# Kernel optimization log

Measured on AMD Instinct MI355X. Metric: run time of the kernel, lower is better.

The kernel has to match this reference:

```python
import jax, jax.numpy as jnp
import numpy as np

B, T, N_POS, N_ACT, H = 256, 512, 128, 32, 512
D = N_POS + N_ACT


def setup_inputs() -> dict:
    key = jax.random.key(0)
    ks = jax.random.split(key, 10)
    s_ih = 1.0 / np.sqrt(H)  # torch LSTMCell default uniform(-1/sqrt(H), 1/sqrt(H))
    xav_hc = np.sqrt(2.0 / (B + H))  # xavier_normal_ on [B,H] h0/c0
    return {
        "observation": jax.random.normal(ks[0], (B, T, N_POS), dtype=jnp.float32),
        "action": jax.random.normal(ks[1], (B, T, N_ACT), dtype=jnp.float32),
        "W_ih": jax.random.uniform(ks[2], (4 * H, D), jnp.float32, -s_ih, s_ih),
        "W_hh": jax.random.uniform(ks[3], (4 * H, H), jnp.float32, -s_ih, s_ih),
        "b_ih": jax.random.uniform(ks[4], (4 * H,), jnp.float32, -s_ih, s_ih),
        "b_hh": jax.random.uniform(ks[5], (4 * H,), jnp.float32, -s_ih, s_ih),
        "W_out": jax.random.uniform(ks[6], (1, H), jnp.float32, -s_ih, s_ih),
        "b_out": jax.random.uniform(ks[7], (1,), jnp.float32, -s_ih, s_ih),
        "h0": jax.random.normal(ks[8], (B, H), dtype=jnp.float32) * xav_hc,
        "c0": jax.random.normal(ks[9], (B, H), dtype=jnp.float32) * xav_hc,
    }


def reference(observation, action, W_ih, W_hh, b_ih, b_hh, W_out, b_out, h0, c0):
    # x: [B,T,D] -> scan over time [T,B,D]
    x = jnp.concatenate([observation, action], axis=-1)
    xs = jnp.transpose(x, (1, 0, 2))
    b = b_ih + b_hh

    def step(carry, x_t):
        h, c = carry
        gates = x_t @ W_ih.T + h @ W_hh.T + b  # [B, 4H]
        i, f, g, o = jnp.split(gates, 4, axis=-1)
        i = jax.nn.sigmoid(i)
        f = jax.nn.sigmoid(f)
        g = jnp.tanh(g)
        o = jax.nn.sigmoid(o)
        c_new = f * c + i * g
        h_new = o * jnp.tanh(c_new)
        y = h_new @ W_out.T + b_out  # [B, 1]
        return (h_new, c_new), y

    _, ys = jax.lax.scan(step, (h0, c0), xs)  # ys: [T, B, 1]
    return jnp.transpose(ys, (1, 0, 2))  # [B, T, 1]
```

## Files before the change

### kernel.cpp

```cpp
#include <hip/hip_runtime.h>
#include <math.h>


namespace {
constexpr int kT = 512, kH = 512;

typedef _Float16 v8h __attribute__((ext_vector_type(8)));
typedef float v4f __attribute__((ext_vector_type(4)));
typedef unsigned long long ull;
typedef ull v2u __attribute__((ext_vector_type(2)));

__device__ __forceinline__ ull ld64sc(const ull* p, bool sys) {
    return sys ? __hip_atomic_load(p, __ATOMIC_RELAXED, __HIP_MEMORY_SCOPE_SYSTEM)
               : __hip_atomic_load(p, __ATOMIC_RELAXED, __HIP_MEMORY_SCOPE_AGENT);
}
__device__ __forceinline__ unsigned ld32sc(const unsigned* p, bool sys) {
    return sys ? __hip_atomic_load(p, __ATOMIC_RELAXED, __HIP_MEMORY_SCOPE_SYSTEM)
               : __hip_atomic_load(p, __ATOMIC_RELAXED, __HIP_MEMORY_SCOPE_AGENT);
}
__device__ __forceinline__ void st32sc(unsigned* p, unsigned v, bool sys) {
    if (sys) __hip_atomic_store(p, v, __ATOMIC_RELAXED, __HIP_MEMORY_SCOPE_SYSTEM);
    else     __hip_atomic_store(p, v, __ATOMIC_RELAXED, __HIP_MEMORY_SCOPE_WORKGROUP);
}
__device__ __forceinline__ unsigned ld_sys32(const unsigned* p) {
    return __hip_atomic_load(p, __ATOMIC_RELAXED, __HIP_MEMORY_SCOPE_SYSTEM);
}

__device__ __forceinline__ float tanhff(float x) {
    return fmaf(-2.0f,
                __builtin_amdgcn_rcpf(__builtin_amdgcn_exp2f(x * 2.885390082f) + 1.0f),
                1.0f);
}

__global__ void lstm_init(const float* __restrict__ h0, _Float16* __restrict__ hfA,
                          unsigned* __restrict__ ctrl) {
    int i = blockIdx.x * blockDim.x + threadIdx.x;
    int bb = i >> 9, j = i & 511;
    int bgrp = bb >> 4, b = bb & 15;
    int ck = j >> 5, jl = j & 31, qf = jl >> 3, e = jl & 7;
    int slot = (qf * 16 + b) ^ ck;
    hfA[bgrp * 8192 + ck * 512 + slot * 8 + e] = (_Float16)h0[i];
    if (i < 1152) ctrl[i] = 0u;
}

__global__ __launch_bounds__(256, 1) void lstm_persist(
    const float* __restrict__ obs, const float* __restrict__ act,
    const float* __restrict__ Wih, const float* __restrict__ Whh,
    const float* __restrict__ bih, const float* __restrict__ bhh,
    const float* __restrict__ Wout, const float* __restrict__ bout_p,
    const float* __restrict__ c0,
    _Float16* __restrict__ hfA, _Float16* __restrict__ hfB,
    unsigned* __restrict__ ctrl, float* __restrict__ out) {

    __shared__ __align__(16) char xbuf[2][5 * 1024];
    __shared__ __align__(16) char hbuf[2][16 * 1024];
    __shared__ float ypart[2][4];
    __shared__ float ytail[2];
    __shared__ int sh_role[3];

    const int tid = threadIdx.x;
    const int w = tid >> 6, ln = tid & 63;
    const int lm = ln & 15, q = ln >> 4;

    unsigned* flags = ctrl;
    unsigned* regcnt = ctrl + 1024;
    unsigned* regtotal = ctrl + 1032;

    if (tid == 0) {
        int x = __builtin_amdgcn_s_getreg(20 | (31 << 11)) & 7;
        unsigned slot = atomicAdd(&regcnt[x], 1u);
        asm volatile("s_waitcnt vmcnt(0)" ::: "memory");
        atomicAdd(regtotal, 1u);
        while (ld_sys32(regtotal) < 256u) __builtin_amdgcn_s_sleep(8);
        unsigned cnt[8];
#pragma unroll
        for (int i = 0; i < 8; ++i) cnt[i] = ld_sys32(&regcnt[i]);
        int pure_base = 0, total_pure = 0, lbase = 0;
        for (int i = 0; i < 8; ++i) {
            if (i < x) { pure_base += cnt[i] >> 4; lbase += cnt[i] & 15; }
            total_pure += cnt[i] >> 4;
        }
        int px16 = (int)(cnt[x] >> 4) * 16;
        int bg, jv, sv;
        if ((int)slot < px16) {
            bg = pure_base + ((int)slot >> 4); jv = slot & 15; sv = 0;
        } else {
            int lr = lbase + ((int)slot - px16);
            bg = total_pure + (lr >> 4); jv = lr & 15; sv = 1;
        }
        sh_role[0] = bg; sh_role[1] = jv; sh_role[2] = sv;
    }
    __syncthreads();
    const int bgrp = sh_role[0], jg = sh_role[1];
    const bool sysS = sh_role[2] != 0;
    const int yb = bgrp * 16 + jg;
    unsigned* myflags = flags + bgrp * 64;

    v8h afrag[2][21];
    {
        const int jj = lm >> 2, gt = lm & 3;
        const float scg = (gt == 2) ? 2.885390082f : -1.442695041f;
#pragma unroll
        for (int ti = 0; ti < 2; ++ti) {
            const int grow = gt * kH + jg * 32 + w * 8 + jj * 2 + ti;
#pragma unroll
            for (int kc = 0; kc < 21; ++kc) {
                const int k0 = kc * 32 + q * 8;
                const float* src = (k0 < 160) ? (Wih + grow * 160 + k0)
                                              : (Whh + (size_t)grow * kH + (k0 - 160));
                float4 A = *(const float4*)src;
                float4 Bv = *(const float4*)(src + 4);
                v8h f;
                f[0] = (_Float16)(A.x * scg);  f[1] = (_Float16)(A.y * scg);
                f[2] = (_Float16)(A.z * scg);  f[3] = (_Float16)(A.w * scg);
                f[4] = (_Float16)(Bv.x * scg); f[5] = (_Float16)(Bv.y * scg);
                f[6] = (_Float16)(Bv.z * scg); f[7] = (_Float16)(Bv.w * scg);
                afrag[ti][kc] = f;
            }
        }
    }
    float biasv[2][4];
    float creg[2];
#pragma unroll
    for (int ti = 0; ti < 2; ++ti) {
        const int jloc = jg * 32 + w * 8 + q * 2 + ti;
#pragma unroll
        for (int g = 0; g < 4; ++g) {
            const float s = (g == 2) ? 2.885390082f : -1.442695041f;
            biasv[ti][g] = (bih[g * kH + jloc] + bhh[g * kH + jloc]) * s;
        }
        creg[ti] = c0[(size_t)(bgrp * 16 + lm) * kH + jloc];
    }

    const float bout0 = bout_p[0];
    const float2 wout2 = *(const float2*)(Wout + 2 * tid);
    float4 wout4 = make_float4(0.f, 0.f, 0.f, 0.f);
    if (tid < 128) wout4 = *(const float4*)(Wout + tid * 4);

    const int st = tid - 96, xb = st & 15, c10 = st >> 4;
    const bool isX = (tid >= 96);
    float4 xr[4];

    auto x_load = [&](int tt) {
        if (isX) {
            const size_t brow = (size_t)(bgrp * 16 + xb) * kT + tt;
            const float* p = (c10 < 8) ? (obs + brow * 128 + c10 * 16)
                                       : (act + brow * 32 + (c10 - 8) * 16);
            xr[0] = *(const float4*)(p);
            xr[1] = *(const float4*)(p + 4);
            xr[2] = *(const float4*)(p + 8);
            xr[3] = *(const float4*)(p + 12);
        }
    };
    auto x_write = [&](char* xbase) {
        if (isX) {
            const int kcx = c10 >> 1;
#pragma unroll
            for (int ii = 0; ii < 2; ++ii) {
                const int qx = (2 * c10 + ii) & 3;
                const int slot = (qx * 16 + xb) ^ kcx;
                float4 a = xr[2 * ii], b = xr[2 * ii + 1];
                v8h f;
                f[0] = (_Float16)a.x; f[1] = (_Float16)a.y;
                f[2] = (_Float16)a.z; f[3] = (_Float16)a.w;
                f[4] = (_Float16)b.x; f[5] = (_Float16)b.y;
                f[6] = (_Float16)b.z; f[7] = (_Float16)b.w;
                *(v8h*)(xbase + kcx * 1024 + slot * 16) = f;
            }
        }
    };

    x_load(0);
    x_write(xbuf[0]);
    x_load(1);
    __syncthreads();

    char* const hfAc = (char*)hfA;
    char* const hfBc = (char*)hfB;

#pragma unroll 1
    for (int t = 0; t < kT; ++t) {
        const char* hsrcB = ((t & 1) ? hfBc : hfAc) + (size_t)bgrp * 16384;
        char* hdstB = ((t & 1) ? hfAc : hfBc) + (size_t)bgrp * 16384;
        const char* xcur = xbuf[t & 1];
        char* hreg = hbuf[t & 1];

        if (t > 0) {
            const unsigned tgt = (unsigned)t;
            const unsigned* fp = myflags + ln;
            unsigned v = ld32sc(fp, sysS);
            while (true) {
                unsigned vn = ld32sc(fp, sysS);
                if (__all((int)(v >= tgt))) break;
                v = vn;
            }
        }

        ull u[8];
#pragma unroll
        for (int k = 0; k < 4; ++k) {
            const ull* sp = (const ull*)(hsrcB + k * 4096 + tid * 16);
            u[2 * k]     = ld64sc(sp, sysS);
            u[2 * k + 1] = ld64sc(sp + 1, sysS);
        }

        v4f a0 = {biasv[0][0], biasv[0][1], biasv[0][2], biasv[0][3]};
        v4f a1 = {biasv[1][0], biasv[1][1], biasv[1][2], biasv[1][3]};
#pragma unroll
        for (int kc = 0; kc < 5; ++kc) {
            v8h bfr = *(const v8h*)(xcur + kc * 1024 + (ln ^ kc) * 16);
            a0 = __builtin_amdgcn_mfma_f32_16x16x32_f16(afrag[0][kc], bfr, a0, 0, 0, 0);
            a1 = __builtin_amdgcn_mfma_f32_16x16x32_f16(afrag[1][kc], bfr, a1, 0, 0, 0);
        }

#pragma unroll
        for (int k = 0; k < 4; ++k) {
            v2u val = {u[2 * k], u[2 * k + 1]};
            *(v2u*)(hreg + k * 4096 + tid * 16) = val;
        }
        if (t < kT - 1) x_write(xbuf[(t + 1) & 1]);
        __syncthreads();

        v4f b0 = {0.f, 0.f, 0.f, 0.f}, b1 = {0.f, 0.f, 0.f, 0.f};
#pragma unroll
        for (int ck = 0; ck < 8; ++ck) {
            v8h bfr = *(const v8h*)(hreg + ck * 1024 + (ln ^ ck) * 16);
            a0 = __builtin_amdgcn_mfma_f32_16x16x32_f16(afrag[0][5 + ck], bfr, a0, 0, 0, 0);
            a1 = __builtin_amdgcn_mfma_f32_16x16x32_f16(afrag[1][5 + ck], bfr, a1, 0, 0, 0);
        }
#pragma unroll
        for (int ck = 8; ck < 16; ++ck) {
            v8h bfr = *(const v8h*)(hreg + ck * 1024 + (ln ^ ck) * 16);
            b0 = __builtin_amdgcn_mfma_f32_16x16x32_f16(afrag[0][5 + ck], bfr, b0, 0, 0, 0);
            b1 = __builtin_amdgcn_mfma_f32_16x16x32_f16(afrag[1][5 + ck], bfr, b1, 0, 0, 0);
        }

        union { unsigned u32; _Float16 h2[2]; } pk;
#pragma unroll
        for (int ti = 0; ti < 2; ++ti) {
            v4f a = ti ? (a1 + b1) : (a0 + b0);
            float iv = __builtin_amdgcn_rcpf(1.0f + __builtin_amdgcn_exp2f(a[0]));
            float fv = __builtin_amdgcn_rcpf(1.0f + __builtin_amdgcn_exp2f(a[1]));
            float gv = fmaf(-2.0f,
                            __builtin_amdgcn_rcpf(__builtin_amdgcn_exp2f(a[2]) + 1.0f),
                            1.0f);
            float ov = __builtin_amdgcn_rcpf(1.0f + __builtin_amdgcn_exp2f(a[3]));
            creg[ti] = fmaf(fv, creg[ti], iv * gv);
            pk.h2[ti] = (_Float16)(ov * tanhff(creg[ti]));
        }
        st32sc((unsigned*)(hdstB + jg * 1024 + (w * 16 + (lm ^ jg)) * 16 + q * 4),
               pk.u32, sysS);

        unsigned yraw = 0;
        if (t > 0) {
            const int k = 2 * tid;
            const int ck = k >> 5, qy = (k >> 3) & 3, e = k & 7;
            const int slot = (qy * 16 + jg) ^ ck;
            yraw = *(const unsigned*)(hreg + ck * 1024 + slot * 16 + e * 2);
        }

        asm volatile("s_waitcnt vmcnt(0)" ::: "memory");
        if (ln == 0) st32sc(myflags + jg * 4 + w, (unsigned)(t + 1), sysS);

        if (t < kT - 2) x_load(t + 2);
        if (t > 0) {
            union { unsigned uu; _Float16 hh[2]; } cv;
            cv.uu = yraw;
            float p = (float)cv.hh[0] * wout2.x + (float)cv.hh[1] * wout2.y;
#pragma unroll
            for (int s = 32; s; s >>= 1) p += __shfl_xor(p, s);
            if (ln == 0) ypart[t & 1][w] = p;
        }
        if (t >= 2 && tid == 64) {
            const float* yp = ypart[(t - 1) & 1];
            out[(size_t)yb * kT + (t - 2)] = bout0 + yp[0] + yp[1] + yp[2] + yp[3];
        }
    }

    if (tid < 64) {
        const unsigned* fp = myflags + ln;
        while (true) {
            unsigned v = ld32sc(fp, sysS);
            if (__all((int)(v >= (unsigned)kT))) break;
            __builtin_amdgcn_s_sleep(1);
        }
    }
    __syncthreads();
    if (tid == 64) {
        const float* yp = ypart[1];
        out[(size_t)yb * kT + (kT - 2)] = bout0 + yp[0] + yp[1] + yp[2] + yp[3];
    }
    if (tid < 128) {
        const int j0 = tid * 4;
        const int ck = j0 >> 5, qf = (j0 >> 3) & 3, e0 = j0 & 7;
        const int slot = (qf * 16 + jg) ^ ck;
        union { ull uu; _Float16 h4[4]; } cv;
        cv.uu = ld64sc((const ull*)(hfAc + (size_t)bgrp * 16384 + ck * 1024 +
                                    slot * 16 + e0 * 2), sysS);
        float p = (float)cv.h4[0] * wout4.x + (float)cv.h4[1] * wout4.y +
                  (float)cv.h4[2] * wout4.z + (float)cv.h4[3] * wout4.w;
#pragma unroll
        for (int s = 32; s; s >>= 1) p += __shfl_xor(p, s);
        if (ln == 0) ytail[w] = p;
    }
    __syncthreads();
    if (tid == 0) out[(size_t)yb * kT + (kT - 1)] = ytail[0] + ytail[1] + bout0;
}

}

extern "C" void kernel_launch(void* const* d_in, const int* in_sizes, int n_in,
                              void* d_out, int out_size, void* d_ws, size_t ws_size,
                              hipStream_t stream) {
    const float* obs  = (const float*)d_in[0];
    const float* act  = (const float*)d_in[1];
    const float* Wih  = (const float*)d_in[2];
    const float* Whh  = (const float*)d_in[3];
    const float* bih  = (const float*)d_in[4];
    const float* bhh  = (const float*)d_in[5];
    const float* Wout = (const float*)d_in[6];
    const float* bout = (const float*)d_in[7];
    const float* h0   = (const float*)d_in[8];
    const float* c0   = (const float*)d_in[9];
    float* out = (float*)d_out;

    char* ws = (char*)d_ws;
    _Float16* hfA = (_Float16*)ws;
    _Float16* hfB = (_Float16*)(ws + 262144);
    unsigned* ctrl = (unsigned*)(ws + 524288);

    lstm_init<<<512, 256, 0, stream>>>(h0, hfA, ctrl);
    lstm_persist<<<256, 256, 0, stream>>>(obs, act, Wih, Whh, bih, bhh, Wout, bout,
                                          c0, hfA, hfB, ctrl, out);
}
```

Measured before the change: 1.327 ms.

## Halve persistent blocks, each computing 64 hidden units per batch group

The persistent LSTM kernel now launches 128 workgroups instead of 256. Each block owns 64 hidden units (four MFMA tiles per wave instead of two) and 8 blocks per batch group instead of 16. This cuts the number of flags polled per step and the number of blocks that must synchronise each timestep, at the cost of double the MFMA work and register pressure per block. The h-state stores become 64-bit, and the output projection is split across two batch rows per block.

```diff
diff --git a/kernel.cpp b/kernel.cpp
--- a/kernel.cpp
+++ b/kernel.cpp
@@ -19,6 +19,10 @@
                : __hip_atomic_load(p, __ATOMIC_RELAXED, __HIP_MEMORY_SCOPE_AGENT);
 }
 __device__ __forceinline__ void st32sc(unsigned* p, unsigned v, bool sys) {
+    if (sys) __hip_atomic_store(p, v, __ATOMIC_RELAXED, __HIP_MEMORY_SCOPE_SYSTEM);
+    else     __hip_atomic_store(p, v, __ATOMIC_RELAXED, __HIP_MEMORY_SCOPE_WORKGROUP);
+}
+__device__ __forceinline__ void st64sc(ull* p, ull v, bool sys) {
     if (sys) __hip_atomic_store(p, v, __ATOMIC_RELAXED, __HIP_MEMORY_SCOPE_SYSTEM);
     else     __hip_atomic_store(p, v, __ATOMIC_RELAXED, __HIP_MEMORY_SCOPE_WORKGROUP);
 }
@@ -55,7 +59,7 @@
     __shared__ __align__(16) char xbuf[2][5 * 1024];
     __shared__ __align__(16) char hbuf[2][16 * 1024];
     __shared__ float ypart[2][4];
-    __shared__ float ytail[2];
+    __shared__ float ytail[4];
     __shared__ int sh_role[3];
 
     const int tid = threadIdx.x;
@@ -71,38 +75,38 @@
         unsigned slot = atomicAdd(&regcnt[x], 1u);
         asm volatile("s_waitcnt vmcnt(0)" ::: "memory");
         atomicAdd(regtotal, 1u);
-        while (ld_sys32(regtotal) < 256u) __builtin_amdgcn_s_sleep(8);
+        while (ld_sys32(regtotal) < 128u) __builtin_amdgcn_s_sleep(8);
         unsigned cnt[8];
 #pragma unroll
         for (int i = 0; i < 8; ++i) cnt[i] = ld_sys32(&regcnt[i]);
         int pure_base = 0, total_pure = 0, lbase = 0;
         for (int i = 0; i < 8; ++i) {
-            if (i < x) { pure_base += cnt[i] >> 4; lbase += cnt[i] & 15; }
-            total_pure += cnt[i] >> 4;
-        }
-        int px16 = (int)(cnt[x] >> 4) * 16;
+            if (i < x) { pure_base += cnt[i] >> 3; lbase += cnt[i] & 7; }
+            total_pure += cnt[i] >> 3;
+        }
+        int px8 = (int)(cnt[x] >> 3) * 8;
         int bg, jv, sv;
-        if ((int)slot < px16) {
-            bg = pure_base + ((int)slot >> 4); jv = slot & 15; sv = 0;
+        if ((int)slot < px8) {
+            bg = pure_base + ((int)slot >> 3); jv = slot & 7; sv = 0;
         } else {
-            int lr = lbase + ((int)slot - px16);
-            bg = total_pure + (lr >> 4); jv = lr & 15; sv = 1;
+            int lr = lbase + ((int)slot - px8);
+            bg = total_pure + (lr >> 3); jv = lr & 7; sv = 1;
         }
         sh_role[0] = bg; sh_role[1] = jv; sh_role[2] = sv;
     }
     __syncthreads();
     const int bgrp = sh_role[0], jg = sh_role[1];
     const bool sysS = sh_role[2] != 0;
-    const int yb = bgrp * 16 + jg;
+    const int yb0 = bgrp * 16 + jg * 2;
     unsigned* myflags = flags + bgrp * 64;
 
-    v8h afrag[2][21];
+    v8h afrag[4][21];
     {
         const int jj = lm >> 2, gt = lm & 3;
         const float scg = (gt == 2) ? 2.885390082f : -1.442695041f;
 #pragma unroll
-        for (int ti = 0; ti < 2; ++ti) {
-            const int grow = gt * kH + jg * 32 + w * 8 + jj * 2 + ti;
+        for (int ti = 0; ti < 4; ++ti) {
+            const int grow = gt * kH + jg * 64 + w * 16 + jj * 4 + ti;
 #pragma unroll
             for (int kc = 0; kc < 21; ++kc) {
                 const int k0 = kc * 32 + q * 8;
@@ -119,11 +123,11 @@
             }
         }
     }
-    float biasv[2][4];
-    float creg[2];
-#pragma unroll
-    for (int ti = 0; ti < 2; ++ti) {
-        const int jloc = jg * 32 + w * 8 + q * 2 + ti;
+    v4f biasv[4];
+    float creg[4];
+#pragma unroll
+    for (int ti = 0; ti < 4; ++ti) {
+        const int jloc = jg * 64 + w * 16 + q * 4 + ti;
 #pragma unroll
         for (int g = 0; g < 4; ++g) {
             const float s = (g == 2) ? 2.885390082f : -1.442695041f;
@@ -133,9 +137,13 @@
     }
 
     const float bout0 = bout_p[0];
-    const float2 wout2 = *(const float2*)(Wout + 2 * tid);
-    float4 wout4 = make_float4(0.f, 0.f, 0.f, 0.f);
-    if (tid < 128) wout4 = *(const float4*)(Wout + tid * 4);
+    const int j0y = (w & 1) * 256 + ln * 4;
+    const int cky = j0y >> 5, jly = j0y & 31;
+    const int oy = cky * 1024 +
+                   ((((jly >> 3) * 16 + (jg * 2 + (w >> 1))) ^ cky) * 16) +
+                   (jly & 7) * 2;
+    const float4 ywt4 = *(const float4*)(Wout + j0y);
+    const float4 wout4 = *(const float4*)(Wout + (tid & 127) * 4);
 
     const int st = tid - 96, xb = st & 15, c10 = st >> 4;
     const bool isX = (tid >= 96);
@@ -178,6 +186,10 @@
     char* const hfAc = (char*)hfA;
     char* const hfBc = (char*)hfB;
 
+    const int ckp = jg * 2 + (w >> 1);
+    const int qfp = (w & 1) * 2 + (q >> 1);
+    const int pofs = ckp * 1024 + (((qfp * 16 + lm) ^ ckp) * 16) + (q & 1) * 8;
+
 #pragma unroll 1
     for (int t = 0; t < kT; ++t) {
         const char* hsrcB = ((t & 1) ? hfBc : hfAc) + (size_t)bgrp * 16384;
@@ -187,7 +199,7 @@
 
         if (t > 0) {
             const unsigned tgt = (unsigned)t;
-            const unsigned* fp = myflags + ln;
+            const unsigned* fp = myflags + (ln & 31);
             unsigned v = ld32sc(fp, sysS);
             while (true) {
                 unsigned vn = ld32sc(fp, sysS);
@@ -204,13 +216,19 @@
             u[2 * k + 1] = ld64sc(sp + 1, sysS);
         }
 
-        v4f a0 = {biasv[0][0], biasv[0][1], biasv[0][2], biasv[0][3]};
-        v4f a1 = {biasv[1][0], biasv[1][1], biasv[1][2], biasv[1][3]};
+        v4f aacc[4], bacc[4];
+#pragma unroll
+        for (int ti = 0; ti < 4; ++ti) {
+            aacc[ti] = biasv[ti];
+            bacc[ti] = v4f{0.f, 0.f, 0.f, 0.f};
+        }
 #pragma unroll
         for (int kc = 0; kc < 5; ++kc) {
             v8h bfr = *(const v8h*)(xcur + kc * 1024 + (ln ^ kc) * 16);
-            a0 = __builtin_amdgcn_mfma_f32_16x16x32_f16(afrag[0][kc], bfr, a0, 0, 0, 0);
-            a1 = __builtin_amdgcn_mfma_f32_16x16x32_f16(afrag[1][kc], bfr, a1, 0, 0, 0);
+#pragma unroll
+            for (int ti = 0; ti < 4; ++ti)
+                aacc[ti] = __builtin_amdgcn_mfma_f32_16x16x32_f16(
+                    afrag[ti][kc], bfr, aacc[ti], 0, 0, 0);
         }
 
 #pragma unroll
@@ -221,24 +239,26 @@
         if (t < kT - 1) x_write(xbuf[(t + 1) & 1]);
         __syncthreads();
 
-        v4f b0 = {0.f, 0.f, 0.f, 0.f}, b1 = {0.f, 0.f, 0.f, 0.f};
-#pragma unroll
-        for (int ck = 0; ck < 8; ++ck) {
+#pragma unroll
+        for (int ck = 0; ck < 16; ++ck) {
             v8h bfr = *(const v8h*)(hreg + ck * 1024 + (ln ^ ck) * 16);
-            a0 = __builtin_amdgcn_mfma_f32_16x16x32_f16(afrag[0][5 + ck], bfr, a0, 0, 0, 0);
-            a1 = __builtin_amdgcn_mfma_f32_16x16x32_f16(afrag[1][5 + ck], bfr, a1, 0, 0, 0);
-        }
-#pragma unroll
-        for (int ck = 8; ck < 16; ++ck) {
-            v8h bfr = *(const v8h*)(hreg + ck * 1024 + (ln ^ ck) * 16);
-            b0 = __builtin_amdgcn_mfma_f32_16x16x32_f16(afrag[0][5 + ck], bfr, b0, 0, 0, 0);
-            b1 = __builtin_amdgcn_mfma_f32_16x16x32_f16(afrag[1][5 + ck], bfr, b1, 0, 0, 0);
-        }
-
-        union { unsigned u32; _Float16 h2[2]; } pk;
-#pragma unroll
-        for (int ti = 0; ti < 2; ++ti) {
-            v4f a = ti ? (a1 + b1) : (a0 + b0);
+            if (ck < 8) {
+#pragma unroll
+                for (int ti = 0; ti < 4; ++ti)
+                    aacc[ti] = __builtin_amdgcn_mfma_f32_16x16x32_f16(
+                        afrag[ti][5 + ck], bfr, aacc[ti], 0, 0, 0);
+            } else {
+#pragma unroll
+                for (int ti = 0; ti < 4; ++ti)
+                    bacc[ti] = __builtin_amdgcn_mfma_f32_16x16x32_f16(
+                        afrag[ti][5 + ck], bfr, bacc[ti], 0, 0, 0);
+            }
+        }
+
+        union { ull u64; _Float16 h4[4]; } pk;
+#pragma unroll
+        for (int ti = 0; ti < 4; ++ti) {
+            v4f a = aacc[ti] + bacc[ti];
             float iv = __builtin_amdgcn_rcpf(1.0f + __builtin_amdgcn_exp2f(a[0]));
             float fv = __builtin_amdgcn_rcpf(1.0f + __builtin_amdgcn_exp2f(a[1]));
             float gv = fmaf(-2.0f,
@@ -246,39 +266,38 @@
                             1.0f);
             float ov = __builtin_amdgcn_rcpf(1.0f + __builtin_amdgcn_exp2f(a[3]));
             creg[ti] = fmaf(fv, creg[ti], iv * gv);
-            pk.h2[ti] = (_Float16)(ov * tanhff(creg[ti]));
-        }
-        st32sc((unsigned*)(hdstB + jg * 1024 + (w * 16 + (lm ^ jg)) * 16 + q * 4),
-               pk.u32, sysS);
-
-        unsigned yraw = 0;
-        if (t > 0) {
-            const int k = 2 * tid;
-            const int ck = k >> 5, qy = (k >> 3) & 3, e = k & 7;
-            const int slot = (qy * 16 + jg) ^ ck;
-            yraw = *(const unsigned*)(hreg + ck * 1024 + slot * 16 + e * 2);
-        }
+            pk.h4[ti] = (_Float16)(ov * tanhff(creg[ti]));
+        }
+        st64sc((ull*)(hdstB + pofs), pk.u64, sysS);
+
+        ull yraw = 0;
+        if (t > 0) yraw = *(const ull*)(hreg + oy);
 
         asm volatile("s_waitcnt vmcnt(0)" ::: "memory");
         if (ln == 0) st32sc(myflags + jg * 4 + w, (unsigned)(t + 1), sysS);
 
         if (t < kT - 2) x_load(t + 2);
         if (t > 0) {
-            union { unsigned uu; _Float16 hh[2]; } cv;
+            union { ull uu; _Float16 hh[4]; } cv;
             cv.uu = yraw;
-            float p = (float)cv.hh[0] * wout2.x + (float)cv.hh[1] * wout2.y;
+            float p = (float)cv.hh[0] * ywt4.x + (float)cv.hh[1] * ywt4.y +
+                      (float)cv.hh[2] * ywt4.z + (float)cv.hh[3] * ywt4.w;
 #pragma unroll
             for (int s = 32; s; s >>= 1) p += __shfl_xor(p, s);
             if (ln == 0) ypart[t & 1][w] = p;
         }
         if (t >= 2 && tid == 64) {
             const float* yp = ypart[(t - 1) & 1];
-            out[(size_t)yb * kT + (t - 2)] = bout0 + yp[0] + yp[1] + yp[2] + yp[3];
+            out[(size_t)yb0 * kT + (t - 2)] = bout0 + yp[0] + yp[1];
+        }
+        if (t >= 2 && tid == 192) {
+            const float* yp = ypart[(t - 1) & 1];
+            out[(size_t)(yb0 + 1) * kT + (t - 2)] = bout0 + yp[2] + yp[3];
         }
     }
 
     if (tid < 64) {
-        const unsigned* fp = myflags + ln;
+        const unsigned* fp = myflags + (ln & 31);
         while (true) {
             unsigned v = ld32sc(fp, sysS);
             if (__all((int)(v >= (unsigned)kT))) break;
@@ -286,14 +305,11 @@
         }
     }
     __syncthreads();
-    if (tid == 64) {
-        const float* yp = ypart[1];
-        out[(size_t)yb * kT + (kT - 2)] = bout0 + yp[0] + yp[1] + yp[2] + yp[3];
-    }
-    if (tid < 128) {
-        const int j0 = tid * 4;
-        const int ck = j0 >> 5, qf = (j0 >> 3) & 3, e0 = j0 & 7;
-        const int slot = (qf * 16 + jg) ^ ck;
+    {
+        const int bsel = jg * 2 + (tid >> 7);
+        const int j0 = (tid & 127) * 4;
+        const int ck = j0 >> 5, jl = j0 & 31, qf = jl >> 3, e0 = jl & 7;
+        const int slot = (qf * 16 + bsel) ^ ck;
         union { ull uu; _Float16 h4[4]; } cv;
         cv.uu = ld64sc((const ull*)(hfAc + (size_t)bgrp * 16384 + ck * 1024 +
                                     slot * 16 + e0 * 2), sysS);
@@ -304,7 +320,18 @@
         if (ln == 0) ytail[w] = p;
     }
     __syncthreads();
-    if (tid == 0) out[(size_t)yb * kT + (kT - 1)] = ytail[0] + ytail[1] + bout0;
+    if (tid == 64) {
+        const float* yp = ypart[1];
+        out[(size_t)yb0 * kT + (kT - 2)] = bout0 + yp[0] + yp[1];
+    }
+    if (tid == 192) {
+        const float* yp = ypart[1];
+        out[(size_t)(yb0 + 1) * kT + (kT - 2)] = bout0 + yp[2] + yp[3];
+    }
+    if (tid == 0) {
+        out[(size_t)yb0 * kT + (kT - 1)] = ytail[0] + ytail[1] + bout0;
+        out[(size_t)(yb0 + 1) * kT + (kT - 1)] = ytail[2] + ytail[3] + bout0;
+    }
 }
 
 }
@@ -330,6 +357,6 @@
     unsigned* ctrl = (unsigned*)(ws + 524288);
 
     lstm_init<<<512, 256, 0, stream>>>(h0, hfA, ctrl);
-    lstm_persist<<<256, 256, 0, stream>>>(obs, act, Wih, Whh, bih, bhh, Wout, bout,
+    lstm_persist<<<128, 256, 0, stream>>>(obs, act, Wih, Whh, bih, bhh, Wout, bout,
                                           c0, hfA, hfB, ctrl, out);
 }
```

Result: slower. 1.807 ms (+36.2%).

## Use 128 persistent blocks of 512 threads, each covering 64 hidden units

Applied to the files above, without the earlier changes.

Restructures the persistent LSTM kernel from 256 blocks of 256 threads to 128 blocks of 512 threads. Each block now owns 64 hidden columns for a 16-batch group, and the XCD registration is regrouped to 8 blocks per batch group. This halves the number of blocks that poll flags and redundantly copy the shared h state per step, cutting inter-block synchronisation and global traffic. In exchange each block has more waves and only 128 CUs are used, and the launch bounds of 512,2 may constrain register use for the large per-thread weight fragments.

```diff
diff --git a/kernel.cpp b/kernel.cpp
--- a/kernel.cpp
+++ b/kernel.cpp
@@ -43,7 +43,7 @@
     if (i < 1152) ctrl[i] = 0u;
 }
 
-__global__ __launch_bounds__(256, 1) void lstm_persist(
+__global__ __launch_bounds__(512, 2) void lstm_persist(
     const float* __restrict__ obs, const float* __restrict__ act,
     const float* __restrict__ Wih, const float* __restrict__ Whh,
     const float* __restrict__ bih, const float* __restrict__ bhh,
@@ -54,8 +54,8 @@
 
     __shared__ __align__(16) char xbuf[2][5 * 1024];
     __shared__ __align__(16) char hbuf[2][16 * 1024];
-    __shared__ float ypart[2][4];
-    __shared__ float ytail[2];
+    __shared__ float ypart[2][8];
+    __shared__ float ytail[4];
     __shared__ int sh_role[3];
 
     const int tid = threadIdx.x;
@@ -71,29 +71,29 @@
         unsigned slot = atomicAdd(&regcnt[x], 1u);
         asm volatile("s_waitcnt vmcnt(0)" ::: "memory");
         atomicAdd(regtotal, 1u);
-        while (ld_sys32(regtotal) < 256u) __builtin_amdgcn_s_sleep(8);
+        while (ld_sys32(regtotal) < 128u) __builtin_amdgcn_s_sleep(8);
         unsigned cnt[8];
 #pragma unroll
         for (int i = 0; i < 8; ++i) cnt[i] = ld_sys32(&regcnt[i]);
         int pure_base = 0, total_pure = 0, lbase = 0;
         for (int i = 0; i < 8; ++i) {
-            if (i < x) { pure_base += cnt[i] >> 4; lbase += cnt[i] & 15; }
-            total_pure += cnt[i] >> 4;
-        }
-        int px16 = (int)(cnt[x] >> 4) * 16;
+            if (i < x) { pure_base += cnt[i] >> 3; lbase += cnt[i] & 7; }
+            total_pure += cnt[i] >> 3;
+        }
+        int px8 = (int)(cnt[x] >> 3) * 8;
         int bg, jv, sv;
-        if ((int)slot < px16) {
-            bg = pure_base + ((int)slot >> 4); jv = slot & 15; sv = 0;
+        if ((int)slot < px8) {
+            bg = pure_base + ((int)slot >> 3); jv = slot & 7; sv = 0;
         } else {
-            int lr = lbase + ((int)slot - px16);
-            bg = total_pure + (lr >> 4); jv = lr & 15; sv = 1;
+            int lr = lbase + ((int)slot - px8);
+            bg = total_pure + (lr >> 3); jv = lr & 7; sv = 1;
         }
         sh_role[0] = bg; sh_role[1] = jv; sh_role[2] = sv;
     }
     __syncthreads();
     const int bgrp = sh_role[0], jg = sh_role[1];
     const bool sysS = sh_role[2] != 0;
-    const int yb = bgrp * 16 + jg;
+    const int yb0 = bgrp * 16 + jg * 2;
     unsigned* myflags = flags + bgrp * 64;
 
     v8h afrag[2][21];
@@ -102,7 +102,7 @@
         const float scg = (gt == 2) ? 2.885390082f : -1.442695041f;
 #pragma unroll
         for (int ti = 0; ti < 2; ++ti) {
-            const int grow = gt * kH + jg * 32 + w * 8 + jj * 2 + ti;
+            const int grow = gt * kH + jg * 64 + w * 8 + jj * 2 + ti;
 #pragma unroll
             for (int kc = 0; kc < 21; ++kc) {
                 const int k0 = kc * 32 + q * 8;
@@ -123,7 +123,7 @@
     float creg[2];
 #pragma unroll
     for (int ti = 0; ti < 2; ++ti) {
-        const int jloc = jg * 32 + w * 8 + q * 2 + ti;
+        const int jloc = jg * 64 + w * 8 + q * 2 + ti;
 #pragma unroll
         for (int g = 0; g < 4; ++g) {
             const float s = (g == 2) ? 2.885390082f : -1.442695041f;
@@ -133,12 +133,16 @@
     }
 
     const float bout0 = bout_p[0];
-    const float2 wout2 = *(const float2*)(Wout + 2 * tid);
+    const int ky = 2 * (tid & 255);
+    const int bloc = jg * 2 + (tid >> 8);
+    const int cky = ky >> 5, jly = ky & 31;
+    const int oy = cky * 1024 + ((((jly >> 3) * 16 + bloc) ^ cky) * 16) + (jly & 7) * 2;
+    const float2 wout2 = *(const float2*)(Wout + ky);
     float4 wout4 = make_float4(0.f, 0.f, 0.f, 0.f);
-    if (tid < 128) wout4 = *(const float4*)(Wout + tid * 4);
+    if (tid < 256) wout4 = *(const float4*)(Wout + (tid & 127) * 4);
 
     const int st = tid - 96, xb = st & 15, c10 = st >> 4;
-    const bool isX = (tid >= 96);
+    const bool isX = (tid >= 96) && (tid < 256);
     float4 xr[4];
 
     auto x_load = [&](int tt) {
@@ -178,6 +182,9 @@
     char* const hfAc = (char*)hfA;
     char* const hfBc = (char*)hfB;
 
+    const int ckp = jg * 2 + (w >> 2);
+    const int pofs = ckp * 1024 + ((((w & 3) * 16 + lm) ^ ckp) * 16) + q * 4;
+
 #pragma unroll 1
     for (int t = 0; t < kT; ++t) {
         const char* hsrcB = ((t & 1) ? hfBc : hfAc) + (size_t)bgrp * 16384;
@@ -196,12 +203,13 @@
             }
         }
 
-        ull u[8];
-#pragma unroll
-        for (int k = 0; k < 4; ++k) {
-            const ull* sp = (const ull*)(hsrcB + k * 4096 + tid * 16);
-            u[2 * k]     = ld64sc(sp, sysS);
-            u[2 * k + 1] = ld64sc(sp + 1, sysS);
+        ull u[4];
+        {
+            const ull* sp = (const ull*)(hsrcB + tid * 32);
+            u[0] = ld64sc(sp + 0, sysS);
+            u[1] = ld64sc(sp + 1, sysS);
+            u[2] = ld64sc(sp + 2, sysS);
+            u[3] = ld64sc(sp + 3, sysS);
         }
 
         v4f a0 = {biasv[0][0], biasv[0][1], biasv[0][2], biasv[0][3]};
@@ -213,10 +221,10 @@
             a1 = __builtin_amdgcn_mfma_f32_16x16x32_f16(afrag[1][kc], bfr, a1, 0, 0, 0);
         }
 
-#pragma unroll
-        for (int k = 0; k < 4; ++k) {
-            v2u val = {u[2 * k], u[2 * k + 1]};
-            *(v2u*)(hreg + k * 4096 + tid * 16) = val;
+        {
+            v2u v0 = {u[0], u[1]}, v1 = {u[2], u[3]};
+            *(v2u*)(hreg + tid * 32) = v0;
+            *(v2u*)(hreg + tid * 32 + 16) = v1;
         }
         if (t < kT - 1) x_write(xbuf[(t + 1) & 1]);
         __syncthreads();
@@ -248,19 +256,13 @@
             creg[ti] = fmaf(fv, creg[ti], iv * gv);
             pk.h2[ti] = (_Float16)(ov * tanhff(creg[ti]));
         }
-        st32sc((unsigned*)(hdstB + jg * 1024 + (w * 16 + (lm ^ jg)) * 16 + q * 4),
-               pk.u32, sysS);
+        st32sc((unsigned*)(hdstB + pofs), pk.u32, sysS);
 
         unsigned yraw = 0;
-        if (t > 0) {
-            const int k = 2 * tid;
-            const int ck = k >> 5, qy = (k >> 3) & 3, e = k & 7;
-            const int slot = (qy * 16 + jg) ^ ck;
-            yraw = *(const unsigned*)(hreg + ck * 1024 + slot * 16 + e * 2);
-        }
+        if (t > 0) yraw = *(const unsigned*)(hreg + oy);
 
         asm volatile("s_waitcnt vmcnt(0)" ::: "memory");
-        if (ln == 0) st32sc(myflags + jg * 4 + w, (unsigned)(t + 1), sysS);
+        if (ln == 0) st32sc(myflags + jg * 8 + w, (unsigned)(t + 1), sysS);
 
         if (t < kT - 2) x_load(t + 2);
         if (t > 0) {
@@ -273,7 +275,11 @@
         }
         if (t >= 2 && tid == 64) {
             const float* yp = ypart[(t - 1) & 1];
-            out[(size_t)yb * kT + (t - 2)] = bout0 + yp[0] + yp[1] + yp[2] + yp[3];
+            out[(size_t)yb0 * kT + (t - 2)] = bout0 + yp[0] + yp[1] + yp[2] + yp[3];
+        }
+        if (t >= 2 && tid == 320) {
+            const float* yp = ypart[(t - 1) & 1];
+            out[(size_t)(yb0 + 1) * kT + (t - 2)] = bout0 + yp[4] + yp[5] + yp[6] + yp[7];
         }
     }
 
@@ -286,14 +292,11 @@
         }
     }
     __syncthreads();
-    if (tid == 64) {
-        const float* yp = ypart[1];
-        out[(size_t)yb * kT + (kT - 2)] = bout0 + yp[0] + yp[1] + yp[2] + yp[3];
-    }
-    if (tid < 128) {
-        const int j0 = tid * 4;
-        const int ck = j0 >> 5, qf = (j0 >> 3) & 3, e0 = j0 & 7;
-        const int slot = (qf * 16 + jg) ^ ck;
+    if (tid < 256) {
+        const int bsel = jg * 2 + (tid >> 7);
+        const int j0 = (tid & 127) * 4;
+        const int ck = j0 >> 5, jl = j0 & 31, qf = jl >> 3, e0 = jl & 7;
+        const int slot = (qf * 16 + bsel) ^ ck;
         union { ull uu; _Float16 h4[4]; } cv;
         cv.uu = ld64sc((const ull*)(hfAc + (size_t)bgrp * 16384 + ck * 1024 +
                                     slot * 16 + e0 * 2), sysS);
@@ -304,7 +307,18 @@
         if (ln == 0) ytail[w] = p;
     }
     __syncthreads();
-    if (tid == 0) out[(size_t)yb * kT + (kT - 1)] = ytail[0] + ytail[1] + bout0;
+    if (tid == 64) {
+        const float* yp = ypart[1];
+        out[(size_t)yb0 * kT + (kT - 2)] = bout0 + yp[0] + yp[1] + yp[2] + yp[3];
+    }
+    if (tid == 320) {
+        const float* yp = ypart[1];
+        out[(size_t)(yb0 + 1) * kT + (kT - 2)] = bout0 + yp[4] + yp[5] + yp[6] + yp[7];
+    }
+    if (tid == 0) {
+        out[(size_t)yb0 * kT + (kT - 1)] = ytail[0] + ytail[1] + bout0;
+        out[(size_t)(yb0 + 1) * kT + (kT - 1)] = ytail[2] + ytail[3] + bout0;
+    }
 }
 
 }
@@ -330,6 +344,6 @@
     unsigned* ctrl = (unsigned*)(ws + 524288);
 
     lstm_init<<<512, 256, 0, stream>>>(h0, hfA, ctrl);
-    lstm_persist<<<256, 256, 0, stream>>>(obs, act, Wih, Whh, bih, bhh, Wout, bout,
+    lstm_persist<<<128, 512, 0, stream>>>(obs, act, Wih, Whh, bih, bhh, Wout, bout,
                                           c0, hfA, hfB, ctrl, out);
 }
```

Measured after the change: 1.390 ms. +4.8%, slower.
